# Kernel tuning notes

Hardware: AMD Instinct MI355X
Metric: run time of the kernel (lower is better)

The kernel has to match this reference:

```python
import jax, jax.numpy as jnp
import numpy as np

HIDDEN = 128
NUM_RADIAL = 16
NUM_DENSE = 3
OUT_DIM = 1
N_NODES = 50000
N_EDGES = 600000


def setup_inputs() -> dict:
    key = jax.random.key(0)
    ks = jax.random.split(key, 16)
    h = jax.random.normal(ks[0], (N_NODES, HIDDEN), dtype=jnp.float32)
    radial_basis = jax.random.normal(ks[1], (N_EDGES, NUM_RADIAL), dtype=jnp.float32)
    edge_index = jax.random.randint(ks[2], (2, N_EDGES), 0, N_NODES, dtype=jnp.int32)

    def lin(k, fan_in, fan_out):
        bound = 1.0 / np.sqrt(fan_in)
        kw, kb = jax.random.split(k)
        W = jax.random.uniform(kw, (fan_in, fan_out), minval=-bound, maxval=bound, dtype=jnp.float32)
        b = jax.random.uniform(kb, (fan_out,), minval=-bound, maxval=bound, dtype=jnp.float32)
        return W, b

    rW1, rb1 = lin(ks[3], NUM_RADIAL, HIDDEN)
    rW2, rb2 = lin(ks[4], HIDDEN, HIDDEN)
    dW, db = [], []
    for i in range(NUM_DENSE):
        W, b = lin(ks[5 + i], HIDDEN, HIDDEN)
        dW.append(W); db.append(b)
    oW, ob = lin(ks[10], HIDDEN, OUT_DIM)
    return {
        "h": h, "radial_basis": radial_basis, "edge_index": edge_index,
        "rW1": rW1, "rb1": rb1, "rW2": rW2, "rb2": rb2,
        "dW0": dW[0], "db0": db[0], "dW1": dW[1], "db1": db[1], "dW2": dW[2], "db2": db[2],
        "oW": oW, "ob": ob,
    }


def reference(h, radial_basis, edge_index, rW1, rb1, rW2, rb2,
              dW0, db0, dW1, db1, dW2, db2, oW, ob):
    src, dst = edge_index[0], edge_index[1]
    # radial_net: Linear -> SiLU -> Linear, output [n_edges, hidden]
    W = jax.nn.silu(radial_basis @ rW1 + rb1) @ rW2 + rb2
    # gather -> multiply -> scatter-add (message passing)
    h_edge = h[src] * W                      # [n_edges, hidden]
    x = jax.ops.segment_sum(h_edge, dst, num_segments=h.shape[0])  # [n_atoms, hidden]
    # dense layers
    for dw, dbias in ((dW0, db0), (dW1, db1), (dW2, db2)):
        x = jax.nn.silu(x @ dw + dbias)
    return x @ oW + ob                        # [n_atoms, output_dim]
```

## Files before the change

kernel.cpp:

```cpp
#include <hip/hip_runtime.h>

typedef short bf16x8 __attribute__((ext_vector_type(8)));
typedef float f32x4 __attribute__((ext_vector_type(4)));
typedef float f32x2 __attribute__((ext_vector_type(2)));
typedef unsigned int u32x4 __attribute__((ext_vector_type(4)));

__device__ __forceinline__ unsigned short f2bf(float f) {
  unsigned int u = __float_as_uint(f);
  u = (u + 0x7FFFu + ((u >> 16) & 1u)) >> 16;
  return (unsigned short)u;
}
__device__ __forceinline__ float bf2f(unsigned short u) {
  return __uint_as_float(((unsigned int)u) << 16);
}
__device__ __forceinline__ float silu_f(float v) {
  return v * (1.0f / (1.0f + __expf(-v)));
}
__device__ __forceinline__ unsigned int pkbf(float a, float b) {
  unsigned int r;
  asm("v_cvt_pk_bf16_f32 %0, %1, %2" : "=v"(r) : "v"(a), "v"(b));
  return r;
}
__device__ __forceinline__ void st2bf(char* base, int byA, int byB, float a, float b) {
  unsigned int p = pkbf(a, b);
  *(unsigned short*)(base + byA) = (unsigned short)p;
  *(unsigned short*)(base + byB) = (unsigned short)(p >> 16);
}

__global__ void k_prep(const float* __restrict__ rW1, const float* __restrict__ rb1,
                       const float* __restrict__ rW2, const float* __restrict__ dW0,
                       const float* __restrict__ dW1, const float* __restrict__ dW2,
                       unsigned short* __restrict__ wb, int* __restrict__ hist,
                       int nzero) {
  int i = blockIdx.x * blockDim.x + threadIdx.x;
  if (i < 4096) {
    int j = i & 7, lane = (i >> 3) & 63, nt = i >> 9;
    int k = (lane >> 4) * 8 + j, n = nt * 16 + (lane & 15);
    float v = (k < 16) ? rW1[k * 128 + n] : (k == 16 ? rb1[n] : 0.0f);
    wb[i] = f2bf(v);
  } else if (i < 4096 + 4 * 16384) {
    int i2 = i - 4096, buf = i2 >> 14, r = i2 & 16383;
    int j = r & 7, lane = (r >> 3) & 63, g = r >> 9, kc = g & 3, nt = g >> 2;
    int k = kc * 32 + (lane >> 4) * 8 + j, n = nt * 16 + (lane & 15);
    const float* W = (buf == 0) ? rW2 : (buf == 1) ? dW0 : (buf == 2) ? dW1 : dW2;
    wb[4096 + buf * 16384 + r] = f2bf(W[k * 128 + n]);
  } else if (i - 69632 < nzero) {
    hist[i - 69632] = 0;
  }
}

__global__ void k_hist(const int* __restrict__ ei, int* __restrict__ hist, int E) {
  int e = blockIdx.x * blockDim.x + threadIdx.x;
  if (e < E) atomicAdd(&hist[ei[E + e]], 1);
}

__global__ __launch_bounds__(1024) void k_scanA(const int* __restrict__ hist,
                                                int* __restrict__ part, int N) {
  __shared__ int red[1024];
  const int t = threadIdx.x;
  const int i = blockIdx.x * 1024 + t;
  red[t] = (i < N) ? hist[i] : 0;
  __syncthreads();
  for (int o = 512; o; o >>= 1) {
    if (t < o) red[t] += red[t + o];
    __syncthreads();
  }
  if (t == 0) part[blockIdx.x] = red[0];
}

__global__ __launch_bounds__(1024) void k_scanC(
    const int* __restrict__ hist, const int* __restrict__ part,
    int* __restrict__ row_start, int* __restrict__ bump, int N, int nb) {
  __shared__ int sh[1024];
  __shared__ int s_off;
  const int t = threadIdx.x;
  const int b = blockIdx.x;
  if (t < 64) {
    int p = (t < nb) ? part[t] : 0;
#pragma unroll
    for (int o = 1; o < 64; o <<= 1) {
      int u = __shfl_up(p, o);
      if (t >= o) p += u;
    }
    if (b == 0) {
      if (t == 0) s_off = 0;
    } else if (t == b - 1) {
      s_off = p;
    }
  }
  __syncthreads();
  const int i = b * 1024 + t;
  const int v = (i < N) ? hist[i] : 0;
  sh[t] = v;
  __syncthreads();
  for (int o = 1; o < 1024; o <<= 1) {
    int u = (t >= o) ? sh[t - o] : 0;
    __syncthreads();
    sh[t] += u;
    __syncthreads();
  }
  const int excl = s_off + sh[t] - v;
  if (i < N) {
    row_start[i] = excl;
    bump[i] = excl;
  } else if (i == N) {
    row_start[N] = excl;
  }
}

__global__ __launch_bounds__(256, 3) void k_edge2(
    const float* __restrict__ rb, const int* __restrict__ ei,
    const float* __restrict__ h, const unsigned short* __restrict__ B1,
    const unsigned short* __restrict__ B2, const float* __restrict__ rb2,
    int* __restrict__ bump, unsigned short* __restrict__ Mbuf,
    int E, int ntiles) {
  const int tid = threadIdx.x;
  const int lane = tid & 63;
  const int wid = tid >> 6;
  const int kg = lane >> 4;
  const int c15 = lane & 15;
  __shared__ __align__(16) unsigned short hid[64 * 128];
  __shared__ __align__(16) unsigned short B2s[16384];

#pragma unroll
  for (int i = 0; i < 8; ++i) {
    const int c = tid + i * 256;
    *(bf16x8*)(B2s + (c << 3)) = *(const bf16x8*)(B2 + (c << 3));
  }
  __syncthreads();

  float rb2r[8];
#pragma unroll
  for (int nt = 0; nt < 8; ++nt) rb2r[nt] = rb2[nt * 16 + c15];

  for (int t = blockIdx.x; t < ntiles; t += gridDim.x) {
    const int ebase = t * 64 + wid * 16;

    int sP[2], pP[2];
#pragma unroll
    for (int pass = 0; pass < 2; ++pass) {
      const int ro8 = pass * 8 + (lane >> 3);
      const int e2 = t * 64 + wid * 16 + ro8;
      int pc = 0;
      sP[pass] = 0;
      if (e2 < E) {
        sP[pass] = ei[e2];
        const int d = ei[E + e2];
        if ((lane & 7) == 0) pc = atomicAdd(&bump[d], 1);
      }
      pP[pass] = __shfl(pc, lane & 56);
    }

    bf16x8 a1 = {};
    if (kg < 2) {
      const int e = ebase + c15;
      if (e < E) {
        const f32x4 v0 = __builtin_nontemporal_load((const f32x4*)(rb + (size_t)e * 16 + kg * 8));
        const f32x4 v1 = __builtin_nontemporal_load((const f32x4*)(rb + (size_t)e * 16 + kg * 8 + 4));
        unsigned int p0 = pkbf(v0[0], v0[1]), p1 = pkbf(v0[2], v0[3]);
        unsigned int p2 = pkbf(v1[0], v1[1]), p3 = pkbf(v1[2], v1[3]);
        a1[0] = (short)(p0 & 0xffff); a1[1] = (short)(p0 >> 16);
        a1[2] = (short)(p1 & 0xffff); a1[3] = (short)(p1 >> 16);
        a1[4] = (short)(p2 & 0xffff); a1[5] = (short)(p2 >> 16);
        a1[6] = (short)(p3 & 0xffff); a1[7] = (short)(p3 >> 16);
      }
    } else if (kg == 2) {
      a1[0] = (short)0x3F80;
    }

#pragma unroll
    for (int nt = 0; nt < 8; ++nt) {
      bf16x8 b1 = *(const bf16x8*)(B1 + ((nt * 64 + lane) << 3));
      f32x4 d1 = {};
      d1 = __builtin_amdgcn_mfma_f32_16x16x32_bf16(a1, b1, d1, 0, 0, 0);
#pragma unroll
      for (int r = 0; r < 4; r += 2) {
        const int row0 = wid * 16 + kg * 4 + r;
        const int row1 = row0 + 1;
        const int col2 = (nt * 16 + c15) * 2;
        st2bf((char*)hid,
              (row0 * 256 + col2) ^ ((row0 & 7) << 4),
              (row1 * 256 + col2) ^ ((row1 & 7) << 4),
              silu_f(d1[r]), silu_f(d1[r + 1]));
      }
    }

    const int arow = wid * 16 + c15;
    f32x4 acc[8] = {};
#pragma unroll
    for (int kc = 0; kc < 4; ++kc) {
      int byt = arow * 256 + (kc * 32 + kg * 8) * 2;
      byt ^= (arow & 7) << 4;
      const bf16x8 a2 = *(const bf16x8*)((const char*)hid + byt);
#pragma unroll
      for (int nt = 0; nt < 8; ++nt) {
        const bf16x8 bf = *(const bf16x8*)(B2s + (((nt * 4 + kc) * 64 + lane) << 3));
        acc[nt] = __builtin_amdgcn_mfma_f32_16x16x32_bf16(a2, bf, acc[nt], 0, 0, 0);
      }
    }

#pragma unroll
    for (int nt = 0; nt < 8; ++nt)
#pragma unroll
      for (int r = 0; r < 4; r += 2) {
        const int row0 = wid * 16 + kg * 4 + r;
        const int row1 = row0 + 1;
        const int col2 = (nt * 16 + c15) * 2;
        st2bf((char*)hid,
              (row0 * 256 + col2) ^ ((row0 & 7) << 4),
              (row1 * 256 + col2) ^ ((row1 & 7) << 4),
              acc[nt][r] + rb2r[nt], acc[nt][r + 1] + rb2r[nt]);
      }

#pragma unroll
    for (int pass = 0; pass < 2; ++pass) {
      const int ro = wid * 16 + pass * 8 + (lane >> 3);
      const int e = t * 64 + ro;
      if (e < E) {
        const int p = pP[pass];
        const int s = sP[pass];
        const int cg = (lane & 7) * 16;
        const int swz = (ro & 7) << 4;
        const int bas = ro * 256 + cg * 2;
        const bf16x8 w0 = *(const bf16x8*)((const char*)hid + (bas ^ swz));
        const bf16x8 w1 = *(const bf16x8*)((const char*)hid + ((bas + 16) ^ swz));
        const f32x4* hp = (const f32x4*)(h + (size_t)s * 128 + cg);
        const f32x4 h0 = hp[0], h1 = hp[1], h2 = hp[2], h3 = hp[3];
        u32x4 m0, m1;
        m0[0] = pkbf(bf2f((unsigned short)w0[0]) * h0[0], bf2f((unsigned short)w0[1]) * h0[1]);
        m0[1] = pkbf(bf2f((unsigned short)w0[2]) * h0[2], bf2f((unsigned short)w0[3]) * h0[3]);
        m0[2] = pkbf(bf2f((unsigned short)w0[4]) * h1[0], bf2f((unsigned short)w0[5]) * h1[1]);
        m0[3] = pkbf(bf2f((unsigned short)w0[6]) * h1[2], bf2f((unsigned short)w0[7]) * h1[3]);
        m1[0] = pkbf(bf2f((unsigned short)w1[0]) * h2[0], bf2f((unsigned short)w1[1]) * h2[1]);
        m1[1] = pkbf(bf2f((unsigned short)w1[2]) * h2[2], bf2f((unsigned short)w1[3]) * h2[3]);
        m1[2] = pkbf(bf2f((unsigned short)w1[4]) * h3[0], bf2f((unsigned short)w1[5]) * h3[1]);
        m1[3] = pkbf(bf2f((unsigned short)w1[6]) * h3[2], bf2f((unsigned short)w1[7]) * h3[3]);
        *(u32x4*)(Mbuf + (size_t)p * 128 + cg) = m0;
        *(u32x4*)(Mbuf + (size_t)p * 128 + cg + 8) = m1;
      }
    }
  }
}

__device__ __forceinline__ void dense_silu_layer(
    unsigned short* xt, const unsigned short* __restrict__ W,
    const float* __restrict__ bias, int wid, int kg, int c15, int lane) {
  const int arow = wid * 16 + c15;
  f32x4 acc[8] = {};
#pragma unroll
  for (int kc = 0; kc < 4; ++kc) {
    int byt = arow * 256 + (kc * 32 + kg * 8) * 2;
    byt ^= (arow & 7) << 4;
    const bf16x8 a2 = *(const bf16x8*)((const char*)xt + byt);
#pragma unroll
    for (int nt = 0; nt < 8; ++nt) {
      const bf16x8 bf = *(const bf16x8*)(W + (((nt * 4 + kc) * 64 + lane) << 3));
      acc[nt] = __builtin_amdgcn_mfma_f32_16x16x32_bf16(a2, bf, acc[nt], 0, 0, 0);
    }
  }
#pragma unroll
  for (int nt = 0; nt < 8; ++nt) {
    const float b = bias[nt * 16 + c15];
#pragma unroll
    for (int r = 0; r < 4; r += 2) {
      const int row0 = wid * 16 + kg * 4 + r;
      const int row1 = row0 + 1;
      const int col2 = (nt * 16 + c15) * 2;
      st2bf((char*)xt,
            (row0 * 256 + col2) ^ ((row0 & 7) << 4),
            (row1 * 256 + col2) ^ ((row1 & 7) << 4),
            silu_f(acc[nt][r] + b), silu_f(acc[nt][r + 1] + b));
    }
  }
}

__global__ __launch_bounds__(512) void k_gtile(
    const unsigned short* __restrict__ Mbuf, const int* __restrict__ row_start,
    const unsigned short* __restrict__ Dw, const float* __restrict__ db0,
    const float* __restrict__ db1, const float* __restrict__ db2,
    const float* __restrict__ oW, const float* __restrict__ ob,
    float* __restrict__ out, int NN, int tiles) {
  const int tid = threadIdx.x;
  const int lane = tid & 63;
  const int wid = tid >> 6;
  const int kg = lane >> 4;
  const int c15 = lane & 15;
  __shared__ __align__(16) unsigned short xt[128 * 128];

  for (int t = blockIdx.x; t < tiles; t += gridDim.x) {
    if (t != (int)blockIdx.x) __syncthreads();
    const int rbase = wid * 16;
    const int nbase = t * 128 + rbase;

    for (int i = 0; i < 16; i += 4) {
      int base[4], len[4];
#pragma unroll
      for (int j = 0; j < 4; ++j) {
        const int n = nbase + i + j;
        if (n < NN) {
          const int b0 = row_start[n];
          base[j] = b0;
          len[j] = row_start[n + 1] - b0;
        } else {
          base[j] = 0;
          len[j] = 0;
        }
      }
      int maxlen = len[0] > len[1] ? len[0] : len[1];
      maxlen = maxlen > len[2] ? maxlen : len[2];
      maxlen = maxlen > len[3] ? maxlen : len[3];
      float s[4][8] = {};
      for (int off = kg; off < maxlen; off += 4) {
#pragma unroll
        for (int j = 0; j < 4; ++j) {
          if (off < len[j]) {
            const bf16x8 v = *(const bf16x8*)(Mbuf + (size_t)(base[j] + off) * 128 + c15 * 8);
#pragma unroll
            for (int k = 0; k < 8; ++k) s[j][k] += bf2f((unsigned short)v[k]);
          }
        }
      }
#pragma unroll
      for (int j = 0; j < 4; ++j)
#pragma unroll
        for (int k = 0; k < 8; ++k) {
          float v = s[j][k];
          v += __shfl_xor(v, 16);
          v += __shfl_xor(v, 32);
          s[j][k] = v;
        }
#pragma unroll
      for (int j = 0; j < 4; ++j) {
        if (kg == j) {
          const int n = nbase + i + j;
          if (n < NN) {
            const int row = rbase + i + j;
            u32x4 w;
            w[0] = pkbf(s[j][0], s[j][1]);
            w[1] = pkbf(s[j][2], s[j][3]);
            w[2] = pkbf(s[j][4], s[j][5]);
            w[3] = pkbf(s[j][6], s[j][7]);
            const int byt = (row * 256 + c15 * 16) ^ ((row & 7) << 4);
            *(u32x4*)((char*)xt + byt) = w;
          }
        }
      }
    }

    __syncthreads();

    dense_silu_layer(xt, Dw, db0, wid, kg, c15, lane);
    dense_silu_layer(xt, Dw + 16384, db1, wid, kg, c15, lane);

    {
      const int arow = wid * 16 + c15;
      const unsigned short* W = Dw + 32768;
      f32x4 acc[8] = {};
#pragma unroll
      for (int kc = 0; kc < 4; ++kc) {
        int byt = arow * 256 + (kc * 32 + kg * 8) * 2;
        byt ^= (arow & 7) << 4;
        const bf16x8 a2 = *(const bf16x8*)((const char*)xt + byt);
#pragma unroll
        for (int nt = 0; nt < 8; ++nt) {
          const bf16x8 bf = *(const bf16x8*)(W + (((nt * 4 + kc) * 64 + lane) << 3));
          acc[nt] = __builtin_amdgcn_mfma_f32_16x16x32_bf16(a2, bf, acc[nt], 0, 0, 0);
        }
      }
      const float obv = ob[0];
#pragma unroll
      for (int r = 0; r < 4; ++r) {
        float p = 0.f;
#pragma unroll
        for (int nt = 0; nt < 8; ++nt) {
          const float b = db2[nt * 16 + c15];
          p += silu_f(acc[nt][r] + b) * oW[nt * 16 + c15];
        }
        p += __shfl_xor(p, 1);
        p += __shfl_xor(p, 2);
        p += __shfl_xor(p, 4);
        p += __shfl_xor(p, 8);
        const int n = nbase + kg * 4 + r;
        if (c15 == 0 && n < NN) out[n] = p + obv;
      }
    }
  }
}

__global__ __launch_bounds__(256, 2) void k_edge(
    const float* __restrict__ rb, const int* __restrict__ ei,
    const float* __restrict__ h, const unsigned short* __restrict__ B1,
    const unsigned short* __restrict__ B2, const float* __restrict__ rb2,
    float* __restrict__ x, int E, int ntiles) {
  const int lane = threadIdx.x & 63;
  const int wid = threadIdx.x >> 6;
  const int kg = lane >> 4;
  const int c15 = lane & 15;
  __shared__ __align__(16) unsigned short hid[64 * 128];

  bf16x8 b2f[8][4];
#pragma unroll
  for (int nt = 0; nt < 8; ++nt)
#pragma unroll
    for (int kc = 0; kc < 4; ++kc)
      b2f[nt][kc] = *(const bf16x8*)(B2 + (((nt * 4 + kc) * 64 + lane) << 3));

  float rb2r[8];
#pragma unroll
  for (int nt = 0; nt < 8; ++nt) rb2r[nt] = rb2[nt * 16 + c15];

  for (int t = blockIdx.x; t < ntiles; t += gridDim.x) {
    const int ebase = t * 64 + wid * 16;
    bf16x8 a1 = {};
    if (kg < 2) {
      const int e = ebase + c15;
      if (e < E) {
        const f32x4 v0 = *(const f32x4*)(rb + (size_t)e * 16 + kg * 8);
        const f32x4 v1 = *(const f32x4*)(rb + (size_t)e * 16 + kg * 8 + 4);
        a1[0] = (short)f2bf(v0[0]); a1[1] = (short)f2bf(v0[1]);
        a1[2] = (short)f2bf(v0[2]); a1[3] = (short)f2bf(v0[3]);
        a1[4] = (short)f2bf(v1[0]); a1[5] = (short)f2bf(v1[1]);
        a1[6] = (short)f2bf(v1[2]); a1[7] = (short)f2bf(v1[3]);
      }
    } else if (kg == 2) {
      a1[0] = (short)0x3F80;
    }
#pragma unroll
    for (int nt = 0; nt < 8; ++nt) {
      bf16x8 b1 = *(const bf16x8*)(B1 + ((nt * 64 + lane) << 3));
      f32x4 d1 = {};
      d1 = __builtin_amdgcn_mfma_f32_16x16x32_bf16(a1, b1, d1, 0, 0, 0);
#pragma unroll
      for (int r = 0; r < 4; ++r) {
        const int row = wid * 16 + kg * 4 + r;
        int byt = row * 256 + (nt * 16 + c15) * 2;
        byt ^= (row & 7) << 4;
        *(unsigned short*)((char*)hid + byt) = f2bf(silu_f(d1[r]));
      }
    }
    const int arow = wid * 16 + c15;
    f32x4 acc[8] = {};
#pragma unroll
    for (int kc = 0; kc < 4; ++kc) {
      int byt = arow * 256 + (kc * 32 + kg * 8) * 2;
      byt ^= (arow & 7) << 4;
      const bf16x8 a2 = *(const bf16x8*)((const char*)hid + byt);
#pragma unroll
      for (int nt = 0; nt < 8; ++nt)
        acc[nt] = __builtin_amdgcn_mfma_f32_16x16x32_bf16(a2, b2f[nt][kc], acc[nt], 0, 0, 0);
    }
#pragma unroll
    for (int r = 0; r < 4; ++r) {
      const int e = ebase + kg * 4 + r;
      if (e < E) {
        const int s = ei[e];
        const int d = ei[E + e];
#pragma unroll
        for (int nt = 0; nt < 8; ++nt) {
          const int col = nt * 16 + c15;
          const float w = acc[nt][r] + rb2r[nt];
          const float hv = h[(size_t)s * 128 + col];
          atomicAdd(x + (size_t)d * 128 + col, w * hv);
        }
      }
    }
  }
}

__global__ __launch_bounds__(256, 2) void k_dense(
    float* __restrict__ x, const unsigned short* __restrict__ Bw,
    const float* __restrict__ bias, int M) {
  const int lane = threadIdx.x & 63;
  const int wid = threadIdx.x >> 6;
  const int kg = lane >> 4;
  const int c15 = lane & 15;

  bf16x8 bf[8][4];
#pragma unroll
  for (int nt = 0; nt < 8; ++nt)
#pragma unroll
    for (int kc = 0; kc < 4; ++kc)
      bf[nt][kc] = *(const bf16x8*)(Bw + (((nt * 4 + kc) * 64 + lane) << 3));

  float br[8];
#pragma unroll
  for (int nt = 0; nt < 8; ++nt) br[nt] = bias[nt * 16 + c15];

  const int tiles = (M + 63) >> 6;
  for (int t = blockIdx.x; t < tiles; t += gridDim.x) {
    const int rbase = t * 64 + wid * 16;
    const int row = rbase + c15;
    bf16x8 a[4];
#pragma unroll
    for (int kc = 0; kc < 4; ++kc) {
      bf16x8 az = {};
      if (row < M) {
        const f32x4 v0 = *(const f32x4*)(x + (size_t)row * 128 + kc * 32 + kg * 8);
        const f32x4 v1 = *(const f32x4*)(x + (size_t)row * 128 + kc * 32 + kg * 8 + 4);
        az[0] = (short)f2bf(v0[0]); az[1] = (short)f2bf(v0[1]);
        az[2] = (short)f2bf(v0[2]); az[3] = (short)f2bf(v0[3]);
        az[4] = (short)f2bf(v1[0]); az[5] = (short)f2bf(v1[1]);
        az[6] = (short)f2bf(v1[2]); az[7] = (short)f2bf(v1[3]);
      }
      a[kc] = az;
    }
    f32x4 acc[8] = {};
#pragma unroll
    for (int kc = 0; kc < 4; ++kc)
#pragma unroll
      for (int nt = 0; nt < 8; ++nt)
        acc[nt] = __builtin_amdgcn_mfma_f32_16x16x32_bf16(a[kc], bf[nt][kc], acc[nt], 0, 0, 0);
#pragma unroll
    for (int r = 0; r < 4; ++r) {
      const int orow = rbase + kg * 4 + r;
      if (orow < M) {
#pragma unroll
        for (int nt = 0; nt < 8; ++nt)
          x[(size_t)orow * 128 + nt * 16 + c15] = silu_f(acc[nt][r] + br[nt]);
      }
    }
  }
}

__global__ void k_out(const float* __restrict__ x, const float* __restrict__ oW,
                      const float* __restrict__ ob, float* __restrict__ out, int M) {
  const int lane = threadIdx.x & 63;
  const int w = (int)((blockIdx.x * blockDim.x + threadIdx.x) >> 6);
  const int nw = (int)((gridDim.x * blockDim.x) >> 6);
  const float w0 = oW[lane], w1 = oW[64 + lane];
  const float obv = ob[0];
  for (int row = w; row < M; row += nw) {
    float a = x[(size_t)row * 128 + lane] * w0 + x[(size_t)row * 128 + 64 + lane] * w1;
#pragma unroll
    for (int m = 32; m; m >>= 1) a += __shfl_xor(a, m);
    if (lane == 0) out[row] = a + obv;
  }
}

extern "C" void kernel_launch(void* const* d_in, const int* in_sizes, int n_in,
                              void* d_out, int out_size, void* d_ws, size_t ws_size,
                              hipStream_t stream) {
  const float* h   = (const float*)d_in[0];
  const float* rb  = (const float*)d_in[1];
  const int*   ei  = (const int*)d_in[2];
  const float* rW1 = (const float*)d_in[3];
  const float* rb1 = (const float*)d_in[4];
  const float* rW2 = (const float*)d_in[5];
  const float* rb2 = (const float*)d_in[6];
  const float* dW0 = (const float*)d_in[7];
  const float* db0 = (const float*)d_in[8];
  const float* dW1 = (const float*)d_in[9];
  const float* db1 = (const float*)d_in[10];
  const float* dW2 = (const float*)d_in[11];
  const float* db2 = (const float*)d_in[12];
  const float* oW  = (const float*)d_in[13];
  const float* ob  = (const float*)d_in[14];

  const int NN = in_sizes[0] / 128;
  const int E  = in_sizes[1] / 16;

  char* base = (char*)d_ws;
  size_t off = 0;
  auto alloc = [&](size_t bytes) {
    char* p = base + off;
    off += (bytes + 255) & ~(size_t)255;
    return p;
  };
  float* x            = (float*)alloc((size_t)NN * 128 * 4);
  unsigned short* wb  = (unsigned short*)alloc((size_t)69632 * 2);
  int* row_start      = (int*)alloc((size_t)(NN + 1) * 4);
  int* hist           = (int*)alloc((size_t)NN * 4);
  int* bump           = (int*)alloc((size_t)NN * 4);
  int* part           = (int*)alloc((size_t)64 * 4);
  unsigned short* Mb  = (unsigned short*)alloc((size_t)E * 256);
  const bool fits = off <= ws_size && NN <= 65535;

  const int ntiles = (E + 63) / 64;
  const int gE = (E + 255) / 256;
  const int nb = (NN + 1023) / 1024;

  if (fits) {
    k_prep<<<(69632 + NN + 255) / 256, 256, 0, stream>>>(rW1, rb1, rW2, dW0, dW1,
                                                         dW2, wb, hist, NN);
    k_hist<<<gE, 256, 0, stream>>>(ei, hist, E);
    k_scanA<<<nb, 1024, 0, stream>>>(hist, part, NN);
    k_scanC<<<nb, 1024, 0, stream>>>(hist, part, row_start, bump, NN, nb);
    const int eg = ntiles < 2048 ? ntiles : 2048;
    k_edge2<<<eg, 256, 0, stream>>>(rb, ei, h, wb, wb + 4096, rb2, bump, Mb, E, ntiles);
    const int gt = (NN + 127) / 128;
    k_gtile<<<gt, 512, 0, stream>>>(Mb, row_start, wb + 20480, db0, db1, db2,
                                    oW, ob, (float*)d_out, NN, gt);
  } else {
    k_prep<<<(69632 + 255) / 256, 256, 0, stream>>>(rW1, rb1, rW2, dW0, dW1,
                                                    dW2, wb, hist, 0);
    hipMemsetAsync(x, 0, (size_t)NN * 512, stream);
    const int eg = ntiles < 1024 ? ntiles : 1024;
    k_edge<<<eg, 256, 0, stream>>>(rb, ei, h, wb, wb + 4096, rb2, x, E, ntiles);
    k_dense<<<512, 256, 0, stream>>>(x, wb + 20480, db0, NN);
    k_dense<<<512, 256, 0, stream>>>(x, wb + 36864, db1, NN);
    k_dense<<<512, 256, 0, stream>>>(x, wb + 53248, db2, NN);
    k_out<<<512, 256, 0, stream>>>(x, oW, ob, (float*)d_out, NN);
  }
}
```

Measured before the change: 282.4 us.

## Precompute dst-sorted edge permutation so edge kernel writes messages contiguously

Adds a k_pos kernel that assigns each edge its CSR slot via atomics and records (edge id, src) in a permutation array. The edge kernel then processes edges in sorted-slot order, gathering radial-basis rows through the permutation and writing messages to contiguous Mbuf rows instead of scattered positions. This moves the atomics and the scattered 256-byte message writes out of the MFMA kernel, in exchange for an extra launch, an 8-byte-per-edge array, and gathered rather than streamed radial-basis reads.

```diff
diff --git a/kernel.cpp b/kernel.cpp
--- a/kernel.cpp
+++ b/kernel.cpp
@@ -108,12 +108,22 @@
   }
 }
 
+__global__ void k_pos(const int* __restrict__ ei, int* __restrict__ bump,
+                      int2* __restrict__ esd, int E) {
+  int e = blockIdx.x * blockDim.x + threadIdx.x;
+  if (e < E) {
+    const int s = ei[e];
+    const int d = ei[E + e];
+    const int p = atomicAdd(&bump[d], 1);
+    esd[p] = make_int2(e, s);
+  }
+}
+
 __global__ __launch_bounds__(256, 3) void k_edge2(
-    const float* __restrict__ rb, const int* __restrict__ ei,
+    const float* __restrict__ rb, const int2* __restrict__ esd,
     const float* __restrict__ h, const unsigned short* __restrict__ B1,
     const unsigned short* __restrict__ B2, const float* __restrict__ rb2,
-    int* __restrict__ bump, unsigned short* __restrict__ Mbuf,
-    int E, int ntiles) {
+    unsigned short* __restrict__ Mbuf, int E, int ntiles) {
   const int tid = threadIdx.x;
   const int lane = tid & 63;
   const int wid = tid >> 6;
@@ -134,29 +144,15 @@
   for (int nt = 0; nt < 8; ++nt) rb2r[nt] = rb2[nt * 16 + c15];
 
   for (int t = blockIdx.x; t < ntiles; t += gridDim.x) {
-    const int ebase = t * 64 + wid * 16;
-
-    int sP[2], pP[2];
-#pragma unroll
-    for (int pass = 0; pass < 2; ++pass) {
-      const int ro8 = pass * 8 + (lane >> 3);
-      const int e2 = t * 64 + wid * 16 + ro8;
-      int pc = 0;
-      sP[pass] = 0;
-      if (e2 < E) {
-        sP[pass] = ei[e2];
-        const int d = ei[E + e2];
-        if ((lane & 7) == 0) pc = atomicAdd(&bump[d], 1);
-      }
-      pP[pass] = __shfl(pc, lane & 56);
-    }
+    const int sbase = t * 64 + wid * 16;
 
     bf16x8 a1 = {};
     if (kg < 2) {
-      const int e = ebase + c15;
-      if (e < E) {
-        const f32x4 v0 = __builtin_nontemporal_load((const f32x4*)(rb + (size_t)e * 16 + kg * 8));
-        const f32x4 v1 = __builtin_nontemporal_load((const f32x4*)(rb + (size_t)e * 16 + kg * 8 + 4));
+      const int slot = sbase + c15;
+      if (slot < E) {
+        const int eid = esd[slot].x;
+        const f32x4 v0 = *(const f32x4*)(rb + (size_t)eid * 16 + kg * 8);
+        const f32x4 v1 = *(const f32x4*)(rb + (size_t)eid * 16 + kg * 8 + 4);
         unsigned int p0 = pkbf(v0[0], v0[1]), p1 = pkbf(v0[2], v0[3]);
         unsigned int p2 = pkbf(v1[0], v1[1]), p3 = pkbf(v1[2], v1[3]);
         a1[0] = (short)(p0 & 0xffff); a1[1] = (short)(p0 >> 16);
@@ -215,10 +211,9 @@
 #pragma unroll
     for (int pass = 0; pass < 2; ++pass) {
       const int ro = wid * 16 + pass * 8 + (lane >> 3);
-      const int e = t * 64 + ro;
-      if (e < E) {
-        const int p = pP[pass];
-        const int s = sP[pass];
+      const int slot = t * 64 + ro;
+      if (slot < E) {
+        const int s = esd[slot].y;
         const int cg = (lane & 7) * 16;
         const int swz = (ro & 7) << 4;
         const int bas = ro * 256 + cg * 2;
@@ -235,8 +230,8 @@
         m1[1] = pkbf(bf2f((unsigned short)w1[2]) * h2[2], bf2f((unsigned short)w1[3]) * h2[3]);
         m1[2] = pkbf(bf2f((unsigned short)w1[4]) * h3[0], bf2f((unsigned short)w1[5]) * h3[1]);
         m1[3] = pkbf(bf2f((unsigned short)w1[6]) * h3[2], bf2f((unsigned short)w1[7]) * h3[3]);
-        *(u32x4*)(Mbuf + (size_t)p * 128 + cg) = m0;
-        *(u32x4*)(Mbuf + (size_t)p * 128 + cg + 8) = m1;
+        *(u32x4*)(Mbuf + (size_t)slot * 128 + cg) = m0;
+        *(u32x4*)(Mbuf + (size_t)slot * 128 + cg + 8) = m1;
       }
     }
   }
@@ -572,6 +567,7 @@
   int* hist           = (int*)alloc((size_t)NN * 4);
   int* bump           = (int*)alloc((size_t)NN * 4);
   int* part           = (int*)alloc((size_t)64 * 4);
+  int2* esd           = (int2*)alloc((size_t)E * 8);
   unsigned short* Mb  = (unsigned short*)alloc((size_t)E * 256);
   const bool fits = off <= ws_size && NN <= 65535;
 
@@ -585,8 +581,9 @@
     k_hist<<<gE, 256, 0, stream>>>(ei, hist, E);
     k_scanA<<<nb, 1024, 0, stream>>>(hist, part, NN);
     k_scanC<<<nb, 1024, 0, stream>>>(hist, part, row_start, bump, NN, nb);
+    k_pos<<<gE, 256, 0, stream>>>(ei, bump, esd, E);
     const int eg = ntiles < 2048 ? ntiles : 2048;
-    k_edge2<<<eg, 256, 0, stream>>>(rb, ei, h, wb, wb + 4096, rb2, bump, Mb, E, ntiles);
+    k_edge2<<<eg, 256, 0, stream>>>(rb, esd, h, wb, wb + 4096, rb2, Mb, E, ntiles);
     const int gt = (NN + 127) / 128;
     k_gtile<<<gt, 512, 0, stream>>>(Mb, row_start, wb + 20480, db0, db1, db2,
                                     oW, ob, (float*)d_out, NN, gt);
```

Result: slower. 301.2 us (+6.7%).
